# Kernel tuning notes

Hardware: AMD Instinct MI355X
Metric: run time of the kernel (lower is better)

## Reference

```python
import jax, jax.numpy as jnp
import numpy as np
from jax import lax

_GRAY = jnp.array([0.299, 0.587, 0.114], dtype=jnp.float32)  # cv2 RGB2GRAY weights


def _conv(x, w, b):
    # x: [B,C,H,W], w: [O,I,kh,kw], SAME padding (matches padding=k//2 for odd k)
    y = lax.conv_general_dilated(x, w, (1, 1), 'SAME',
                                 dimension_numbers=('NCHW', 'OIHW', 'NCHW'))
    return y + b[None, :, None, None]


def _maxpool2(x):
    return lax.reduce_window(x, -jnp.inf, lax.max, (1, 1, 2, 2), (1, 1, 2, 2), 'VALID')


def _resize_bilinear(img, out_h, out_w):
    # cv2.resize INTER_LINEAR semantics: half-pixel-centered bilinear sampling, edge clamped
    B, C, H, W = img.shape
    ys = jnp.clip((jnp.arange(out_h, dtype=jnp.float32) + 0.5) * (H / out_h) - 0.5, 0.0, H - 1)
    xs = jnp.clip((jnp.arange(out_w, dtype=jnp.float32) + 0.5) * (W / out_w) - 0.5, 0.0, W - 1)
    y0 = jnp.floor(ys).astype(jnp.int32)
    x0 = jnp.floor(xs).astype(jnp.int32)
    y1 = jnp.minimum(y0 + 1, H - 1)
    x1 = jnp.minimum(x0 + 1, W - 1)
    wy = (ys - y0.astype(jnp.float32))[None, None, :, None]
    wx = (xs - x0.astype(jnp.float32))[None, None, None, :]
    r0 = img[:, :, y0, :]
    r1 = img[:, :, y1, :]
    rows = r0 * (1.0 - wy) + r1 * wy          # [B,C,out_h,W]
    c0 = rows[:, :, :, x0]
    c1 = rows[:, :, :, x1]
    return c0 * (1.0 - wx) + c1 * wx          # [B,C,out_h,out_w]


def _forward(input, w1, b1, w2, b2, w3, b3, w4, b4, w5, b5):
    x = jax.nn.relu(_conv(input, w1, b1))
    x = _maxpool2(x)
    x = jax.nn.relu(_conv(x, w2, b2))
    x = _maxpool2(x)
    x = jax.nn.relu(_conv(x, w3, b3))
    x = jax.nn.relu(_conv(x, w4, b4))
    x = _conv(x, w5, b5)                       # [B,1,H/4,W/4]
    out_h, out_w = x.shape[2], x.shape[3]
    # rgb2gray path is detached in the original (detach().cpu()): stop_gradient
    gray = jnp.einsum('bchw,c->bhw', lax.stop_gradient(input), _GRAY)[:, None]  # [B,1,H,W]
    gray = _resize_bilinear(gray, out_h, out_w)
    return jax.nn.relu(x + jax.nn.relu(gray))


def setup_inputs() -> dict:
    key = jax.random.key(0)
    ks = jax.random.split(key, 12)
    B, H, W = 8, 768, 1024
    def w(k, shape, fan_in):
        return (jax.random.normal(k, shape, dtype=jnp.float32) / np.sqrt(fan_in)).astype(jnp.float32)
    return {
        'input': jax.random.normal(ks[0], (B, 3, H, W), dtype=jnp.float32),
        'w1': w(ks[1], (20, 3, 7, 7), 3 * 49),  'b1': jnp.zeros((20,), jnp.float32),
        'w2': w(ks[2], (40, 20, 5, 5), 20 * 25), 'b2': jnp.zeros((40,), jnp.float32),
        'w3': w(ks[3], (20, 40, 5, 5), 40 * 25), 'b3': jnp.zeros((20,), jnp.float32),
        'w4': w(ks[4], (10, 20, 5, 5), 20 * 25), 'b4': jnp.zeros((10,), jnp.float32),
        'w5': w(ks[5], (1, 10, 1, 1), 10),       'b5': jnp.zeros((1,), jnp.float32),
    }


def reference(input, w1, b1, w2, b2, w3, b3, w4, b4, w5, b5):
    return _forward(input, w1, b1, w2, b2, w3, b3, w4, b4, w5, b5)
```

## Files before the change

kernel.cpp:

```cpp
#include <hip/hip_runtime.h>


typedef _Float16 half_t;
typedef _Float16 half8 __attribute__((ext_vector_type(8)));
typedef float floatx4 __attribute__((ext_vector_type(4)));

#define IN_H 768
#define IN_W 1024
#define P1H 384
#define P1W 512
#define P2H 192
#define P2W 256

#define OFF_P2 0ULL
#define OFF_P1 44040192ULL
#define OFF_X3 44040192ULL
#define OFF_X4 0ULL
#define OFF_W2 119537664ULL
#define OFF_W3 119691264ULL
#define OFF_W4 119896064ULL
#define OFF_W1 119947264ULL

union PK4 { half_t h[4]; uint2 u; };
union U8 { half8 v; uint2 u[2]; };

__global__ __launch_bounds__(256) void pack_weights(
    const float* __restrict__ w2, const float* __restrict__ w3,
    const float* __restrict__ w4, const float* __restrict__ w1,
    half_t* __restrict__ wp2, half_t* __restrict__ wp3, half_t* __restrict__ wp4,
    half_t* __restrict__ wp1)
{
  int t = blockIdx.x * 256 + threadIdx.x;
  if (t < 38400) {
    int tap = t / 1536, r = t % 1536, oc = r >> 5, c = r & 31;
    float v = (oc < 40 && c < 20) ? w2[(oc * 20 + c) * 25 + tap] : 0.f;
    wp2[t] = (half_t)v;
  } else if (t < 89600) {
    int u = t - 38400;
    int tap = u / 2048, r = u % 2048, oc = r >> 6, c = r & 63;
    float v = (oc < 20 && c < 40) ? w3[(oc * 40 + c) * 25 + tap] : 0.f;
    wp3[u] = (half_t)v;
  } else if (t < 102400) {
    int u = t - 89600;
    int tap = u / 512, r = u % 512, oc = r >> 5, c = r & 31;
    float v = (oc < 10 && c < 20) ? w4[(oc * 20 + c) * 25 + tap] : 0.f;
    wp4[u] = (half_t)v;
  } else if (t < 109568) {
    int u = t - 102400;
    int ky = u / 1024, r = u % 1024, oc = r >> 5, k = r & 31;
    int kx = k >> 2, c = k & 3;
    float v = (oc < 20 && c < 3 && kx < 7) ? w1[((oc * 3 + c) * 7 + ky) * 7 + kx] : 0.f;
    wp1[u] = (half_t)v;
  }
}

__global__ __launch_bounds__(256) void conv1_mfma(
    const float* __restrict__ in, const half_t* __restrict__ wp,
    const float* __restrict__ bias, half_t* __restrict__ P1)
{
  __shared__ __align__(16) half_t ltile[38 * 40 * 4];
  const int b = blockIdx.z, ty0 = blockIdx.y * 32, tx0 = blockIdx.x * 32;
  const int tid = threadIdx.x;
  const int HW1 = IN_H * IN_W;

  const float* p0 = in + (size_t)b * 3 * HW1;
  const bool interior = (blockIdx.x >= 1) && (blockIdx.x <= 30) &&
                        (blockIdx.y >= 1) && (blockIdx.y <= 22);
  if (interior) {
    for (int i = tid; i < 380; i += 256) {
      int r = i / 10, c4 = i - r * 10;
      const float* pr = p0 + (size_t)(ty0 - 3 + r) * IN_W + (tx0 - 4 + 4 * c4);
      float4 v0 = *(const float4*)(pr);
      float4 v1 = *(const float4*)(pr + HW1);
      float4 v2 = *(const float4*)(pr + 2 * HW1);
      PK4 a0, a1, a2, a3;
      a0.h[0] = (half_t)v0.x; a0.h[1] = (half_t)v1.x; a0.h[2] = (half_t)v2.x; a0.h[3] = (half_t)0.f;
      a1.h[0] = (half_t)v0.y; a1.h[1] = (half_t)v1.y; a1.h[2] = (half_t)v2.y; a1.h[3] = (half_t)0.f;
      a2.h[0] = (half_t)v0.z; a2.h[1] = (half_t)v1.z; a2.h[2] = (half_t)v2.z; a2.h[3] = (half_t)0.f;
      a3.h[0] = (half_t)v0.w; a3.h[1] = (half_t)v1.w; a3.h[2] = (half_t)v2.w; a3.h[3] = (half_t)0.f;
      uint4* dst = (uint4*)(ltile + (r * 40 + 4 * c4) * 4);
      dst[0] = make_uint4(a0.u.x, a0.u.y, a1.u.x, a1.u.y);
      dst[1] = make_uint4(a2.u.x, a2.u.y, a3.u.x, a3.u.y);
    }
  } else {
    for (int i = tid; i < 1520; i += 256) {
      int r = i / 40, c = i - r * 40;
      int gy = ty0 - 3 + r, gx = tx0 - 4 + c;
      float v0 = 0.f, v1 = 0.f, v2 = 0.f;
      if (gy >= 0 && gy < IN_H && (unsigned)gx < (unsigned)IN_W) {
        size_t o = (size_t)gy * IN_W + gx;
        v0 = p0[o];
        v1 = p0[o + HW1];
        v2 = p0[o + 2 * HW1];
      }
      PK4 pk;
      pk.h[0] = (half_t)v0; pk.h[1] = (half_t)v1;
      pk.h[2] = (half_t)v2; pk.h[3] = (half_t)0.f;
      *(uint2*)(ltile + (r * 40 + c) * 4) = pk.u;
    }
  }
  __syncthreads();

  const int wv = tid >> 6, ln = tid & 63, q = ln >> 4, nl = ln & 15;
  const int cbase = (2 * nl + 2 * q + 1) * 4;
  const half_t* wA = wp + nl * 32 + q * 8;

  floatx4 bv[2];
  #pragma unroll
  for (int mt = 0; mt < 2; ++mt)
    #pragma unroll
    for (int r = 0; r < 4; ++r) {
      int oc = mt * 16 + q * 4 + r;
      bv[mt][r] = (oc < 20) ? bias[oc] : 0.f;
    }
  const int pc = (tx0 >> 1) + nl;

  #pragma unroll
  for (int p = 0; p < 2; ++p) {
    const int rbase = p * 16 + 4 * wv;
    U8 frag[4][2];
    #pragma unroll
    for (int d = 0; d < 4; ++d) {
      const half_t* rp = ltile + (rbase + d) * 160 + cbase;
      #pragma unroll
      for (int phx = 0; phx < 2; ++phx) {
        frag[d][phx].u[0] = *(const uint2*)(rp + phx * 4);
        frag[d][phx].u[1] = *(const uint2*)(rp + phx * 4 + 4);
      }
    }
    half8 Abuf[2][2];
    Abuf[0][0] = *(const half8*)(wA);
    Abuf[0][1] = *(const half8*)(wA + 512);
    floatx4 acc[2][8];
    #pragma unroll
    for (int mt = 0; mt < 2; ++mt)
      #pragma unroll
      for (int j = 0; j < 8; ++j) acc[mt][j] = (floatx4){0.f, 0.f, 0.f, 0.f};

    #pragma unroll
    for (int ky = 0; ky < 7; ++ky) {
      if (ky < 6) {
        Abuf[(ky + 1) & 1][0] = *(const half8*)(wA + (ky + 1) * 1024);
        Abuf[(ky + 1) & 1][1] = *(const half8*)(wA + (ky + 1) * 1024 + 512);
      }
      #pragma unroll
      for (int j = 0; j < 8; ++j) {
        const int g = j >> 2, ph = j & 3, phy = ph >> 1, phx = ph & 1;
        half8 B = frag[(2 * g + phy + ky) & 3][phx].v;
        acc[0][j] = __builtin_amdgcn_mfma_f32_16x16x32_f16(Abuf[ky & 1][0], B, acc[0][j], 0, 0, 0);
        acc[1][j] = __builtin_amdgcn_mfma_f32_16x16x32_f16(Abuf[ky & 1][1], B, acc[1][j], 0, 0, 0);
      }
      if (ky < 6) {
        const half_t* rp = ltile + (rbase + ky + 4) * 160 + cbase;
        #pragma unroll
        for (int phx = 0; phx < 2; ++phx) {
          frag[ky & 3][phx].u[0] = *(const uint2*)(rp + phx * 4);
          frag[ky & 3][phx].u[1] = *(const uint2*)(rp + phx * 4 + 4);
        }
      }
    }

    const int pr0 = (ty0 >> 1) + 8 * p + 2 * wv;
    #pragma unroll
    for (int g = 0; g < 2; ++g) {
      size_t pxbase = (((size_t)b * P1H + pr0 + g) * P1W + pc) * 24;
      PK4 pk0;
      #pragma unroll
      for (int r = 0; r < 4; ++r) {
        float x = fmaxf(fmaxf(acc[0][g * 4 + 0][r], acc[0][g * 4 + 1][r]),
                        fmaxf(acc[0][g * 4 + 2][r], acc[0][g * 4 + 3][r]));
        pk0.h[r] = (half_t)fmaxf(x + bv[0][r], 0.f);
      }
      *(uint2*)(P1 + pxbase + q * 4) = pk0.u;
      if (q < 2) {
        PK4 pk1;
        #pragma unroll
        for (int r = 0; r < 4; ++r) {
          float x = fmaxf(fmaxf(acc[1][g * 4 + 0][r], acc[1][g * 4 + 1][r]),
                          fmaxf(acc[1][g * 4 + 2][r], acc[1][g * 4 + 3][r]));
          pk1.h[r] = (half_t)fmaxf(x + bv[1][r], 0.f);
        }
        *(uint2*)(P1 + pxbase + 16 + q * 4) = pk1.u;
      }
    }
  }
}

__global__ __launch_bounds__(256, 2) void conv2_mfma(
    const half_t* __restrict__ P1, const half_t* __restrict__ wp,
    const float* __restrict__ bias, half_t* __restrict__ P2)
{
  __shared__ __align__(16) half_t lin[20 * 36 * 24 + 16];
  const int b = blockIdx.z, ty0 = blockIdx.y * 16, tx0 = blockIdx.x * 32;
  const int tid = threadIdx.x;
  if (tid < 16) lin[20 * 36 * 24 + tid] = (half_t)0.f;
  for (int i = tid; i < 2160; i += 256) {
    int px = i / 3, part = i - px * 3;
    int row = px / 36, col = px - row * 36;
    int gy = ty0 - 2 + row, gx = tx0 - 2 + col;
    uint4 v = make_uint4(0, 0, 0, 0);
    if (gy >= 0 && gy < P1H && (unsigned)gx < (unsigned)P1W)
      v = *(const uint4*)(P1 + (((size_t)b * P1H + gy) * P1W + gx) * 24 + part * 8);
    *(uint4*)(lin + px * 24 + part * 8) = v;
  }
  __syncthreads();

  const int wv = tid >> 6, ln = tid & 63, q = ln >> 4, nl = ln & 15;
  const int cbase = 2 * nl * 24 + q * 8;
  half8 frag[4][6];
  #pragma unroll
  for (int d = 0; d < 4; ++d) {
    const half_t* rp = lin + (4 * wv + d) * 864 + cbase;
    #pragma unroll
    for (int c = 0; c < 6; ++c) frag[d][c] = *(const half8*)(rp + c * 24);
  }
  const half_t* wA = wp + nl * 32 + q * 8;
  half8 Abuf[2][3];
  #pragma unroll
  for (int mt = 0; mt < 3; ++mt) Abuf[0][mt] = *(const half8*)(wA + mt * 512);
  floatx4 acc[3][8];
  #pragma unroll
  for (int mt = 0; mt < 3; ++mt)
    #pragma unroll
    for (int j = 0; j < 8; ++j) acc[mt][j] = (floatx4){0.f, 0.f, 0.f, 0.f};

  #pragma unroll
  for (int ky = 0; ky < 5; ++ky) {
    #pragma unroll
    for (int kx = 0; kx < 5; ++kx) {
      const int tap = ky * 5 + kx;
      if (tap < 24) {
        #pragma unroll
        for (int mt = 0; mt < 3; ++mt)
          Abuf[(tap + 1) & 1][mt] = *(const half8*)(wA + (tap + 1) * 1536 + mt * 512);
      }
      #pragma unroll
      for (int j = 0; j < 8; ++j) {
        const int g = j >> 2, ph = j & 3, phy = ph >> 1, phx = ph & 1;
        half8 B = frag[(2 * g + phy + ky) & 3][kx + phx];
        acc[0][j] = __builtin_amdgcn_mfma_f32_16x16x32_f16(Abuf[tap & 1][0], B, acc[0][j], 0, 0, 0);
        acc[1][j] = __builtin_amdgcn_mfma_f32_16x16x32_f16(Abuf[tap & 1][1], B, acc[1][j], 0, 0, 0);
        acc[2][j] = __builtin_amdgcn_mfma_f32_16x16x32_f16(Abuf[tap & 1][2], B, acc[2][j], 0, 0, 0);
      }
    }
    if (ky < 4) {
      const half_t* rp = lin + (4 * wv + ky + 4) * 864 + cbase;
      #pragma unroll
      for (int c = 0; c < 6; ++c) frag[ky & 3][c] = *(const half8*)(rp + c * 24);
    }
  }

  floatx4 bv[3];
  #pragma unroll
  for (int mt = 0; mt < 3; ++mt)
    #pragma unroll
    for (int r = 0; r < 4; ++r) {
      int oc = mt * 16 + q * 4 + r;
      bv[mt][r] = (oc < 40) ? bias[oc] : 0.f;
    }
  const int pr0 = (ty0 >> 1) + 2 * wv;
  const int pc = (tx0 >> 1) + nl;
  #pragma unroll
  for (int g = 0; g < 2; ++g) {
    size_t pxbase = (((size_t)b * P2H + pr0 + g) * P2W + pc) * 56;
    #pragma unroll
    for (int mt = 0; mt < 3; ++mt) {
      PK4 pk;
      #pragma unroll
      for (int r = 0; r < 4; ++r) {
        float x = fmaxf(fmaxf(acc[mt][g * 4 + 0][r], acc[mt][g * 4 + 1][r]),
                        fmaxf(acc[mt][g * 4 + 2][r], acc[mt][g * 4 + 3][r]));
        pk.h[r] = (half_t)fmaxf(x + bv[mt][r], 0.f);
      }
      *(uint2*)(P2 + pxbase + mt * 16 + q * 4) = pk.u;
    }
    if (q == 0)
      *(uint4*)(P2 + pxbase + 48) = make_uint4(0, 0, 0, 0);
  }
}

__global__ __launch_bounds__(256, 2) void conv3_mfma(
    const half_t* __restrict__ P2, const half_t* __restrict__ wp,
    const float* __restrict__ bias, half_t* __restrict__ X3)
{
  __shared__ __align__(16) half_t lin[12 * 36 * 56 + 16];
  const int b = blockIdx.z, ty0 = blockIdx.y * 8, tx0 = blockIdx.x * 32;
  const int tid = threadIdx.x;
  if (tid < 16) lin[12 * 36 * 56 + tid] = (half_t)0.f;
  for (int i = tid; i < 3024; i += 256) {
    int px = i / 7, part = i - px * 7;
    int row = px / 36, col = px - row * 36;
    int gy = ty0 - 2 + row, gx = tx0 - 2 + col;
    uint4 v = make_uint4(0, 0, 0, 0);
    if (gy >= 0 && gy < P2H && (unsigned)gx < (unsigned)P2W)
      v = *(const uint4*)(P2 + (((size_t)b * P2H + gy) * P2W + gx) * 56 + part * 8);
    *(uint4*)(lin + px * 56 + part * 8) = v;
  }
  __syncthreads();

  const int wv = tid >> 6, ln = tid & 63, q = ln >> 4, nl = ln & 15;
  const int cbase = 2 * nl * 56 + q * 8;
  half8 frag[2][6][2];
  #pragma unroll
  for (int c = 0; c < 6; ++c)
    #pragma unroll
    for (int cb = 0; cb < 2; ++cb) {
      frag[0][c][cb] = *(const half8*)(lin + (2 * wv + 0) * 2016 + cbase + c * 56 + cb * 32);
      frag[1][c][cb] = *(const half8*)(lin + (2 * wv + 1) * 2016 + cbase + c * 56 + cb * 32);
    }
  const half_t* wA = wp + nl * 64 + q * 8;
  half8 Abuf[2][2][2];
  #pragma unroll
  for (int mt = 0; mt < 2; ++mt)
    #pragma unroll
    for (int cb = 0; cb < 2; ++cb)
      Abuf[0][mt][cb] = *(const half8*)(wA + mt * 1024 + cb * 32);
  floatx4 acc[2][4];
  #pragma unroll
  for (int mt = 0; mt < 2; ++mt)
    #pragma unroll
    for (int j = 0; j < 4; ++j) acc[mt][j] = (floatx4){0.f, 0.f, 0.f, 0.f};

  #pragma unroll
  for (int ky = 0; ky < 5; ++ky) {
    #pragma unroll
    for (int kx = 0; kx < 5; ++kx) {
      const int tap = ky * 5 + kx;
      if (tap < 24) {
        #pragma unroll
        for (int mt = 0; mt < 2; ++mt)
          #pragma unroll
          for (int cb = 0; cb < 2; ++cb)
            Abuf[(tap + 1) & 1][mt][cb] =
                *(const half8*)(wA + (tap + 1) * 2048 + mt * 1024 + cb * 32);
      }
      #pragma unroll
      for (int cb = 0; cb < 2; ++cb)
        #pragma unroll
        for (int j = 0; j < 4; ++j) {
          const int phy = j >> 1, phx = j & 1;
          half8 B = frag[(ky + phy) & 1][kx + phx][cb];
          acc[0][j] = __builtin_amdgcn_mfma_f32_16x16x32_f16(Abuf[tap & 1][0][cb], B, acc[0][j], 0, 0, 0);
          acc[1][j] = __builtin_amdgcn_mfma_f32_16x16x32_f16(Abuf[tap & 1][1][cb], B, acc[1][j], 0, 0, 0);
        }
    }
    if (ky < 4) {
      const half_t* rp = lin + (2 * wv + ky + 2) * 2016 + cbase;
      #pragma unroll
      for (int c = 0; c < 6; ++c)
        #pragma unroll
        for (int cb = 0; cb < 2; ++cb)
          frag[ky & 1][c][cb] = *(const half8*)(rp + c * 56 + cb * 32);
    }
  }

  floatx4 bv[2];
  #pragma unroll
  for (int mt = 0; mt < 2; ++mt)
    #pragma unroll
    for (int r = 0; r < 4; ++r) {
      int oc = mt * 16 + q * 4 + r;
      bv[mt][r] = (oc < 20) ? bias[oc] : 0.f;
    }
  #pragma unroll
  for (int j = 0; j < 4; ++j) {
    const int phy = j >> 1, phx = j & 1;
    int y = ty0 + 2 * wv + phy, x = tx0 + 2 * nl + phx;
    size_t pxbase = (((size_t)b * P2H + y) * P2W + x) * 24;
    #pragma unroll
    for (int mt = 0; mt < 2; ++mt) {
      if (mt == 1 && q >= 2) continue;
      floatx4 v = acc[mt][j];
      PK4 pk;
      #pragma unroll
      for (int r = 0; r < 4; ++r) pk.h[r] = (half_t)fmaxf(v[r] + bv[mt][r], 0.f);
      *(uint2*)(X3 + pxbase + mt * 16 + q * 4) = pk.u;
    }
  }
}

__global__ __launch_bounds__(256, 2) void conv4_mfma(
    const half_t* __restrict__ X3, const half_t* __restrict__ wp,
    const float* __restrict__ bias, float* __restrict__ X4)
{
  __shared__ __align__(16) half_t lin[20 * 36 * 24 + 16];
  const int b = blockIdx.z, ty0 = blockIdx.y * 16, tx0 = blockIdx.x * 32;
  const int tid = threadIdx.x;
  if (tid < 16) lin[20 * 36 * 24 + tid] = (half_t)0.f;
  for (int i = tid; i < 2160; i += 256) {
    int px = i / 3, part = i - px * 3;
    int row = px / 36, col = px - row * 36;
    int gy = ty0 - 2 + row, gx = tx0 - 2 + col;
    uint4 v = make_uint4(0, 0, 0, 0);
    if (gy >= 0 && gy < P2H && (unsigned)gx < (unsigned)P2W)
      v = *(const uint4*)(X3 + (((size_t)b * P2H + gy) * P2W + gx) * 24 + part * 8);
    *(uint4*)(lin + px * 24 + part * 8) = v;
  }
  __syncthreads();

  const int wv = tid >> 6, ln = tid & 63, q = ln >> 4, nl = ln & 15;
  const int cbase = 2 * nl * 24 + q * 8;
  half8 frag[4][6];
  #pragma unroll
  for (int d = 0; d < 4; ++d) {
    const half_t* rp = lin + (4 * wv + d) * 864 + cbase;
    #pragma unroll
    for (int c = 0; c < 6; ++c) frag[d][c] = *(const half8*)(rp + c * 24);
  }
  const half_t* wA = wp + nl * 32 + q * 8;
  half8 Abuf[2];
  Abuf[0] = *(const half8*)(wA);
  floatx4 acc[8];
  #pragma unroll
  for (int j = 0; j < 8; ++j) acc[j] = (floatx4){0.f, 0.f, 0.f, 0.f};

  #pragma unroll
  for (int ky = 0; ky < 5; ++ky) {
    #pragma unroll
    for (int kx = 0; kx < 5; ++kx) {
      const int tap = ky * 5 + kx;
      if (tap < 24) Abuf[(tap + 1) & 1] = *(const half8*)(wA + (tap + 1) * 512);
      #pragma unroll
      for (int j = 0; j < 8; ++j) {
        const int g = j >> 2, ph = j & 3, phy = ph >> 1, phx = ph & 1;
        half8 B = frag[(2 * g + phy + ky) & 3][kx + phx];
        acc[j] = __builtin_amdgcn_mfma_f32_16x16x32_f16(Abuf[tap & 1], B, acc[j], 0, 0, 0);
      }
    }
    if (ky < 4) {
      const half_t* rp = lin + (4 * wv + ky + 4) * 864 + cbase;
      #pragma unroll
      for (int c = 0; c < 6; ++c) frag[ky & 3][c] = *(const half8*)(rp + c * 24);
    }
  }

  float bv[4];
  #pragma unroll
  for (int r = 0; r < 4; ++r) {
    int oc = q * 4 + r;
    bv[r] = (oc < 10) ? bias[oc] : 0.f;
  }
  #pragma unroll
  for (int j = 0; j < 8; ++j) {
    const int g = j >> 2, ph = j & 3, phy = ph >> 1, phx = ph & 1;
    int y = ty0 + 4 * wv + 2 * g + phy, x = tx0 + 2 * nl + phx;
    float* dst = X4 + (((size_t)b * P2H + y) * P2W + x) * 10;
    floatx4 v = acc[j];
    float r0 = fmaxf(v[0] + bv[0], 0.f), r1 = fmaxf(v[1] + bv[1], 0.f);
    float r2 = fmaxf(v[2] + bv[2], 0.f), r3 = fmaxf(v[3] + bv[3], 0.f);
    if (q < 2) {
      *(float2*)(dst + q * 4)     = make_float2(r0, r1);
      *(float2*)(dst + q * 4 + 2) = make_float2(r2, r3);
    } else if (q == 2) {
      *(float2*)(dst + 8) = make_float2(r0, r1);
    }
  }
}

__global__ __launch_bounds__(256) void conv5_res(
    const float* __restrict__ X4, const float* __restrict__ w5,
    const float* __restrict__ b5, const float* __restrict__ in,
    float* __restrict__ out)
{
  const int idx = blockIdx.x * 256 + threadIdx.x;
  const int j = idx & 255;
  const int bi = idx >> 8;
  const int i = bi % 192;
  const int b = bi / 192;
  const float* xp = X4 + (((size_t)b * P2H + i) * P2W + j) * 10;
  float sum = b5[0];
  #pragma unroll
  for (int c = 0; c < 10; ++c) sum += w5[c] * xp[c];
  const int r0 = 4 * i + 1;
  const size_t cb = (size_t)r0 * IN_W + 4 * j;
  float g = 0.f;
  #pragma unroll
  for (int ch = 0; ch < 3; ++ch) {
    const float coef = (ch == 0) ? 0.299f : ((ch == 1) ? 0.587f : 0.114f);
    const float* q = in + ((size_t)b * 3 + ch) * IN_H * IN_W;
    float4 a = *(const float4*)(q + cb);
    float4 d = *(const float4*)(q + cb + IN_W);
    g += coef * (a.y + a.z + d.y + d.z);
  }
  g *= 0.25f;
  out[idx] = fmaxf(sum + fmaxf(g, 0.f), 0.f);
}

extern "C" void kernel_launch(void* const* d_in, const int* in_sizes, int n_in,
                              void* d_out, int out_size, void* d_ws, size_t ws_size,
                              hipStream_t stream) {
  const float* input = (const float*)d_in[0];
  const float* w1 = (const float*)d_in[1];  const float* b1 = (const float*)d_in[2];
  const float* w2 = (const float*)d_in[3];  const float* b2 = (const float*)d_in[4];
  const float* w3 = (const float*)d_in[5];  const float* b3 = (const float*)d_in[6];
  const float* w4 = (const float*)d_in[7];  const float* b4 = (const float*)d_in[8];
  const float* w5 = (const float*)d_in[9];  const float* b5 = (const float*)d_in[10];
  float* out = (float*)d_out;
  char* ws = (char*)d_ws;

  half_t* P2h = (half_t*)(ws + OFF_P2);
  half_t* P1h = (half_t*)(ws + OFF_P1);
  half_t* X3h = (half_t*)(ws + OFF_X3);
  float*  X4f = (float*)(ws + OFF_X4);
  half_t* wp2 = (half_t*)(ws + OFF_W2);
  half_t* wp3 = (half_t*)(ws + OFF_W3);
  half_t* wp4 = (half_t*)(ws + OFF_W4);
  half_t* wp1 = (half_t*)(ws + OFF_W1);

  pack_weights<<<432, 256, 0, stream>>>(w2, w3, w4, w1, wp2, wp3, wp4, wp1);
  conv1_mfma<<<dim3(32, 24, 8), 256, 0, stream>>>(input, wp1, b1, P1h);
  conv2_mfma<<<dim3(16, 24, 8), 256, 0, stream>>>(P1h, wp2, b2, P2h);
  conv3_mfma<<<dim3(8, 24, 8), 256, 0, stream>>>(P2h, wp3, b3, X3h);
  conv4_mfma<<<dim3(8, 12, 8), 256, 0, stream>>>(X3h, wp4, b4, X4f);
  conv5_res<<<1536, 256, 0, stream>>>(X4f, w5, b5, input, out);
}
```

Baseline: 385.3 us.

## Use async global-to-LDS loads with double-buffered multi-tile loops in conv2-4

Replaces the register round-trip staging of halo tiles in conv2, conv3 and conv4 with global_load_lds direct-to-LDS copies. Out-of-bounds lanes read from a small zeroed buffer that pack_weights now fills. conv2 and conv4 now process several row tiles per block (4 and 2) with double-buffered LDS, so the next tile is prefetched while MFMA work runs on the current one. The grids are shrunk to match. The cost is double the LDS per block, which may lower occupancy, and fewer blocks in flight.

```diff
diff --git a/kernel.cpp b/kernel.cpp
--- a/kernel.cpp
+++ b/kernel.cpp
@@ -20,15 +20,21 @@
 #define OFF_W3 119691264ULL
 #define OFF_W4 119896064ULL
 #define OFF_W1 119947264ULL
+#define OFF_ZP 119961600ULL
 
 union PK4 { half_t h[4]; uint2 u; };
 union U8 { half8 v; uint2 u[2]; };
+
+#define GLD16(gsrc, ldst)                                          \
+  __builtin_amdgcn_global_load_lds(                                \
+      (const __attribute__((address_space(1))) void*)(gsrc),       \
+      (__attribute__((address_space(3))) void*)(ldst), 16, 0, 0)
 
 __global__ __launch_bounds__(256) void pack_weights(
     const float* __restrict__ w2, const float* __restrict__ w3,
     const float* __restrict__ w4, const float* __restrict__ w1,
     half_t* __restrict__ wp2, half_t* __restrict__ wp3, half_t* __restrict__ wp4,
-    half_t* __restrict__ wp1)
+    half_t* __restrict__ wp1, half_t* __restrict__ zp)
 {
   int t = blockIdx.x * 256 + threadIdx.x;
   if (t < 38400) {
@@ -51,6 +57,8 @@
     int kx = k >> 2, c = k & 3;
     float v = (oc < 20 && c < 3 && kx < 7) ? w1[((oc * 3 + c) * 7 + ky) * 7 + kx] : 0.f;
     wp1[u] = (half_t)v;
+  } else if (t < 109824) {
+    zp[t - 109568] = (half_t)0.f;
   }
 }
 
@@ -188,68 +196,31 @@
 
 __global__ __launch_bounds__(256, 2) void conv2_mfma(
     const half_t* __restrict__ P1, const half_t* __restrict__ wp,
-    const float* __restrict__ bias, half_t* __restrict__ P2)
+    const float* __restrict__ bias, half_t* __restrict__ P2,
+    const half_t* __restrict__ zp)
 {
-  __shared__ __align__(16) half_t lin[20 * 36 * 24 + 16];
-  const int b = blockIdx.z, ty0 = blockIdx.y * 16, tx0 = blockIdx.x * 32;
+  __shared__ __align__(16) half_t lin[2 * 18432];
+  const int b = blockIdx.z, ty_base = blockIdx.y * 64, tx0 = blockIdx.x * 32;
   const int tid = threadIdx.x;
-  if (tid < 16) lin[20 * 36 * 24 + tid] = (half_t)0.f;
-  for (int i = tid; i < 2160; i += 256) {
-    int px = i / 3, part = i - px * 3;
-    int row = px / 36, col = px - row * 36;
-    int gy = ty0 - 2 + row, gx = tx0 - 2 + col;
-    uint4 v = make_uint4(0, 0, 0, 0);
-    if (gy >= 0 && gy < P1H && (unsigned)gx < (unsigned)P1W)
-      v = *(const uint4*)(P1 + (((size_t)b * P1H + gy) * P1W + gx) * 24 + part * 8);
-    *(uint4*)(lin + px * 24 + part * 8) = v;
-  }
-  __syncthreads();
-
   const int wv = tid >> 6, ln = tid & 63, q = ln >> 4, nl = ln & 15;
+
+  auto stage = [&](int bufsel, int sty0) {
+    half_t* Lb = lin + bufsel * 18432;
+    #pragma unroll
+    for (int r = 0; r < 9; ++r) {
+      int i = r * 256 + tid;
+      int px = i / 3, part = i - px * 3;
+      int row = px / 36, col = px - row * 36;
+      int gy = sty0 - 2 + row, gx = tx0 - 2 + col;
+      const half_t* src = zp;
+      if (i < 2160 && (unsigned)gy < (unsigned)P1H && (unsigned)gx < (unsigned)P1W)
+        src = P1 + (((size_t)b * P1H + gy) * P1W + gx) * 24 + part * 8;
+      GLD16(src, Lb + (size_t)(r * 256 + wv * 64) * 8);
+    }
+  };
+
   const int cbase = 2 * nl * 24 + q * 8;
-  half8 frag[4][6];
-  #pragma unroll
-  for (int d = 0; d < 4; ++d) {
-    const half_t* rp = lin + (4 * wv + d) * 864 + cbase;
-    #pragma unroll
-    for (int c = 0; c < 6; ++c) frag[d][c] = *(const half8*)(rp + c * 24);
-  }
   const half_t* wA = wp + nl * 32 + q * 8;
-  half8 Abuf[2][3];
-  #pragma unroll
-  for (int mt = 0; mt < 3; ++mt) Abuf[0][mt] = *(const half8*)(wA + mt * 512);
-  floatx4 acc[3][8];
-  #pragma unroll
-  for (int mt = 0; mt < 3; ++mt)
-    #pragma unroll
-    for (int j = 0; j < 8; ++j) acc[mt][j] = (floatx4){0.f, 0.f, 0.f, 0.f};
-
-  #pragma unroll
-  for (int ky = 0; ky < 5; ++ky) {
-    #pragma unroll
-    for (int kx = 0; kx < 5; ++kx) {
-      const int tap = ky * 5 + kx;
-      if (tap < 24) {
-        #pragma unroll
-        for (int mt = 0; mt < 3; ++mt)
-          Abuf[(tap + 1) & 1][mt] = *(const half8*)(wA + (tap + 1) * 1536 + mt * 512);
-      }
-      #pragma unroll
-      for (int j = 0; j < 8; ++j) {
-        const int g = j >> 2, ph = j & 3, phy = ph >> 1, phx = ph & 1;
-        half8 B = frag[(2 * g + phy + ky) & 3][kx + phx];
-        acc[0][j] = __builtin_amdgcn_mfma_f32_16x16x32_f16(Abuf[tap & 1][0], B, acc[0][j], 0, 0, 0);
-        acc[1][j] = __builtin_amdgcn_mfma_f32_16x16x32_f16(Abuf[tap & 1][1], B, acc[1][j], 0, 0, 0);
-        acc[2][j] = __builtin_amdgcn_mfma_f32_16x16x32_f16(Abuf[tap & 1][2], B, acc[2][j], 0, 0, 0);
-      }
-    }
-    if (ky < 4) {
-      const half_t* rp = lin + (4 * wv + ky + 4) * 864 + cbase;
-      #pragma unroll
-      for (int c = 0; c < 6; ++c) frag[ky & 3][c] = *(const half8*)(rp + c * 24);
-    }
-  }
-
   floatx4 bv[3];
   #pragma unroll
   for (int mt = 0; mt < 3; ++mt)
@@ -258,47 +229,104 @@
       int oc = mt * 16 + q * 4 + r;
       bv[mt][r] = (oc < 40) ? bias[oc] : 0.f;
     }
-  const int pr0 = (ty0 >> 1) + 2 * wv;
   const int pc = (tx0 >> 1) + nl;
-  #pragma unroll
-  for (int g = 0; g < 2; ++g) {
-    size_t pxbase = (((size_t)b * P2H + pr0 + g) * P2W + pc) * 56;
-    #pragma unroll
-    for (int mt = 0; mt < 3; ++mt) {
-      PK4 pk;
-      #pragma unroll
-      for (int r = 0; r < 4; ++r) {
-        float x = fmaxf(fmaxf(acc[mt][g * 4 + 0][r], acc[mt][g * 4 + 1][r]),
-                        fmaxf(acc[mt][g * 4 + 2][r], acc[mt][g * 4 + 3][r]));
-        pk.h[r] = (half_t)fmaxf(x + bv[mt][r], 0.f);
-      }
-      *(uint2*)(P2 + pxbase + mt * 16 + q * 4) = pk.u;
-    }
-    if (q == 0)
-      *(uint4*)(P2 + pxbase + 48) = make_uint4(0, 0, 0, 0);
+
+  stage(0, ty_base);
+  __syncthreads();
+
+  #pragma unroll 1
+  for (int p = 0; p < 4; ++p) {
+    if (p < 3) stage((p + 1) & 1, ty_base + (p + 1) * 16);
+    const half_t* L = lin + (p & 1) * 18432;
+    const int ty0 = ty_base + p * 16;
+
+    half8 frag[4][6];
+    #pragma unroll
+    for (int d = 0; d < 4; ++d) {
+      const half_t* rp = L + (4 * wv + d) * 864 + cbase;
+      #pragma unroll
+      for (int c = 0; c < 6; ++c) frag[d][c] = *(const half8*)(rp + c * 24);
+    }
+    half8 Abuf[2][3];
+    #pragma unroll
+    for (int mt = 0; mt < 3; ++mt) Abuf[0][mt] = *(const half8*)(wA + mt * 512);
+    floatx4 acc[3][8];
+    #pragma unroll
+    for (int mt = 0; mt < 3; ++mt)
+      #pragma unroll
+      for (int j = 0; j < 8; ++j) acc[mt][j] = (floatx4){0.f, 0.f, 0.f, 0.f};
+
+    #pragma unroll
+    for (int ky = 0; ky < 5; ++ky) {
+      #pragma unroll
+      for (int kx = 0; kx < 5; ++kx) {
+        const int tap = ky * 5 + kx;
+        if (tap < 24) {
+          #pragma unroll
+          for (int mt = 0; mt < 3; ++mt)
+            Abuf[(tap + 1) & 1][mt] = *(const half8*)(wA + (tap + 1) * 1536 + mt * 512);
+        }
+        #pragma unroll
+        for (int j = 0; j < 8; ++j) {
+          const int g = j >> 2, ph = j & 3, phy = ph >> 1, phx = ph & 1;
+          half8 B = frag[(2 * g + phy + ky) & 3][kx + phx];
+          acc[0][j] = __builtin_amdgcn_mfma_f32_16x16x32_f16(Abuf[tap & 1][0], B, acc[0][j], 0, 0, 0);
+          acc[1][j] = __builtin_amdgcn_mfma_f32_16x16x32_f16(Abuf[tap & 1][1], B, acc[1][j], 0, 0, 0);
+          acc[2][j] = __builtin_amdgcn_mfma_f32_16x16x32_f16(Abuf[tap & 1][2], B, acc[2][j], 0, 0, 0);
+        }
+      }
+      if (ky < 4) {
+        const half_t* rp = L + (4 * wv + ky + 4) * 864 + cbase;
+        #pragma unroll
+        for (int c = 0; c < 6; ++c) frag[ky & 3][c] = *(const half8*)(rp + c * 24);
+      }
+    }
+
+    const int pr0 = (ty0 >> 1) + 2 * wv;
+    #pragma unroll
+    for (int g = 0; g < 2; ++g) {
+      size_t pxbase = (((size_t)b * P2H + pr0 + g) * P2W + pc) * 56;
+      #pragma unroll
+      for (int mt = 0; mt < 3; ++mt) {
+        PK4 pk;
+        #pragma unroll
+        for (int r = 0; r < 4; ++r) {
+          float x = fmaxf(fmaxf(acc[mt][g * 4 + 0][r], acc[mt][g * 4 + 1][r]),
+                          fmaxf(acc[mt][g * 4 + 2][r], acc[mt][g * 4 + 3][r]));
+          pk.h[r] = (half_t)fmaxf(x + bv[mt][r], 0.f);
+        }
+        *(uint2*)(P2 + pxbase + mt * 16 + q * 4) = pk.u;
+      }
+      if (q == 0)
+        *(uint4*)(P2 + pxbase + 48) = make_uint4(0, 0, 0, 0);
+    }
+    if (p < 3) __syncthreads();
   }
 }
 
 __global__ __launch_bounds__(256, 2) void conv3_mfma(
     const half_t* __restrict__ P2, const half_t* __restrict__ wp,
-    const float* __restrict__ bias, half_t* __restrict__ X3)
+    const float* __restrict__ bias, half_t* __restrict__ X3,
+    const half_t* __restrict__ zp)
 {
-  __shared__ __align__(16) half_t lin[12 * 36 * 56 + 16];
+  __shared__ __align__(16) half_t lin[24576];
   const int b = blockIdx.z, ty0 = blockIdx.y * 8, tx0 = blockIdx.x * 32;
   const int tid = threadIdx.x;
-  if (tid < 16) lin[12 * 36 * 56 + tid] = (half_t)0.f;
-  for (int i = tid; i < 3024; i += 256) {
+  const int wv = tid >> 6, ln = tid & 63, q = ln >> 4, nl = ln & 15;
+
+  #pragma unroll
+  for (int r = 0; r < 12; ++r) {
+    int i = r * 256 + tid;
     int px = i / 7, part = i - px * 7;
     int row = px / 36, col = px - row * 36;
     int gy = ty0 - 2 + row, gx = tx0 - 2 + col;
-    uint4 v = make_uint4(0, 0, 0, 0);
-    if (gy >= 0 && gy < P2H && (unsigned)gx < (unsigned)P2W)
-      v = *(const uint4*)(P2 + (((size_t)b * P2H + gy) * P2W + gx) * 56 + part * 8);
-    *(uint4*)(lin + px * 56 + part * 8) = v;
+    const half_t* src = zp;
+    if (i < 3024 && (unsigned)gy < (unsigned)P2H && (unsigned)gx < (unsigned)P2W)
+      src = P2 + (((size_t)b * P2H + gy) * P2W + gx) * 56 + part * 8;
+    GLD16(src, lin + (size_t)(r * 256 + wv * 64) * 8);
   }
   __syncthreads();
 
-  const int wv = tid >> 6, ln = tid & 63, q = ln >> 4, nl = ln & 15;
   const int cbase = 2 * nl * 56 + q * 8;
   half8 frag[2][6][2];
   #pragma unroll
@@ -381,79 +409,96 @@
 
 __global__ __launch_bounds__(256, 2) void conv4_mfma(
     const half_t* __restrict__ X3, const half_t* __restrict__ wp,
-    const float* __restrict__ bias, float* __restrict__ X4)
+    const float* __restrict__ bias, float* __restrict__ X4,
+    const half_t* __restrict__ zp)
 {
-  __shared__ __align__(16) half_t lin[20 * 36 * 24 + 16];
-  const int b = blockIdx.z, ty0 = blockIdx.y * 16, tx0 = blockIdx.x * 32;
+  __shared__ __align__(16) half_t lin[2 * 18432];
+  const int b = blockIdx.z, ty_base = blockIdx.y * 32, tx0 = blockIdx.x * 32;
   const int tid = threadIdx.x;
-  if (tid < 16) lin[20 * 36 * 24 + tid] = (half_t)0.f;
-  for (int i = tid; i < 2160; i += 256) {
-    int px = i / 3, part = i - px * 3;
-    int row = px / 36, col = px - row * 36;
-    int gy = ty0 - 2 + row, gx = tx0 - 2 + col;
-    uint4 v = make_uint4(0, 0, 0, 0);
-    if (gy >= 0 && gy < P2H && (unsigned)gx < (unsigned)P2W)
-      v = *(const uint4*)(X3 + (((size_t)b * P2H + gy) * P2W + gx) * 24 + part * 8);
-    *(uint4*)(lin + px * 24 + part * 8) = v;
-  }
-  __syncthreads();
-
   const int wv = tid >> 6, ln = tid & 63, q = ln >> 4, nl = ln & 15;
+
+  auto stage = [&](int bufsel, int sty0) {
+    half_t* Lb = lin + bufsel * 18432;
+    #pragma unroll
+    for (int r = 0; r < 9; ++r) {
+      int i = r * 256 + tid;
+      int px = i / 3, part = i - px * 3;
+      int row = px / 36, col = px - row * 36;
+      int gy = sty0 - 2 + row, gx = tx0 - 2 + col;
+      const half_t* src = zp;
+      if (i < 2160 && (unsigned)gy < (unsigned)P2H && (unsigned)gx < (unsigned)P2W)
+        src = X3 + (((size_t)b * P2H + gy) * P2W + gx) * 24 + part * 8;
+      GLD16(src, Lb + (size_t)(r * 256 + wv * 64) * 8);
+    }
+  };
+
   const int cbase = 2 * nl * 24 + q * 8;
-  half8 frag[4][6];
-  #pragma unroll
-  for (int d = 0; d < 4; ++d) {
-    const half_t* rp = lin + (4 * wv + d) * 864 + cbase;
-    #pragma unroll
-    for (int c = 0; c < 6; ++c) frag[d][c] = *(const half8*)(rp + c * 24);
-  }
   const half_t* wA = wp + nl * 32 + q * 8;
-  half8 Abuf[2];
-  Abuf[0] = *(const half8*)(wA);
-  floatx4 acc[8];
-  #pragma unroll
-  for (int j = 0; j < 8; ++j) acc[j] = (floatx4){0.f, 0.f, 0.f, 0.f};
-
-  #pragma unroll
-  for (int ky = 0; ky < 5; ++ky) {
-    #pragma unroll
-    for (int kx = 0; kx < 5; ++kx) {
-      const int tap = ky * 5 + kx;
-      if (tap < 24) Abuf[(tap + 1) & 1] = *(const half8*)(wA + (tap + 1) * 512);
-      #pragma unroll
-      for (int j = 0; j < 8; ++j) {
-        const int g = j >> 2, ph = j & 3, phy = ph >> 1, phx = ph & 1;
-        half8 B = frag[(2 * g + phy + ky) & 3][kx + phx];
-        acc[j] = __builtin_amdgcn_mfma_f32_16x16x32_f16(Abuf[tap & 1], B, acc[j], 0, 0, 0);
-      }
-    }
-    if (ky < 4) {
-      const half_t* rp = lin + (4 * wv + ky + 4) * 864 + cbase;
-      #pragma unroll
-      for (int c = 0; c < 6; ++c) frag[ky & 3][c] = *(const half8*)(rp + c * 24);
-    }
-  }
-
   float bv[4];
   #pragma unroll
   for (int r = 0; r < 4; ++r) {
     int oc = q * 4 + r;
     bv[r] = (oc < 10) ? bias[oc] : 0.f;
   }
-  #pragma unroll
-  for (int j = 0; j < 8; ++j) {
-    const int g = j >> 2, ph = j & 3, phy = ph >> 1, phx = ph & 1;
-    int y = ty0 + 4 * wv + 2 * g + phy, x = tx0 + 2 * nl + phx;
-    float* dst = X4 + (((size_t)b * P2H + y) * P2W + x) * 10;
-    floatx4 v = acc[j];
-    float r0 = fmaxf(v[0] + bv[0], 0.f), r1 = fmaxf(v[1] + bv[1], 0.f);
-    float r2 = fmaxf(v[2] + bv[2], 0.f), r3 = fmaxf(v[3] + bv[3], 0.f);
-    if (q < 2) {
-      *(float2*)(dst + q * 4)     = make_float2(r0, r1);
-      *(float2*)(dst + q * 4 + 2) = make_float2(r2, r3);
-    } else if (q == 2) {
-      *(float2*)(dst + 8) = make_float2(r0, r1);
-    }
+
+  stage(0, ty_base);
+  __syncthreads();
+
+  #pragma unroll 1
+  for (int p = 0; p < 2; ++p) {
+    if (p < 1) stage(1, ty_base + 16);
+    const half_t* L = lin + (p & 1) * 18432;
+    const int ty0 = ty_base + p * 16;
+
+    half8 frag[4][6];
+    #pragma unroll
+    for (int d = 0; d < 4; ++d) {
+      const half_t* rp = L + (4 * wv + d) * 864 + cbase;
+      #pragma unroll
+      for (int c = 0; c < 6; ++c) frag[d][c] = *(const half8*)(rp + c * 24);
+    }
+    half8 Abuf[2];
+    Abuf[0] = *(const half8*)(wA);
+    floatx4 acc[8];
+    #pragma unroll
+    for (int j = 0; j < 8; ++j) acc[j] = (floatx4){0.f, 0.f, 0.f, 0.f};
+
+    #pragma unroll
+    for (int ky = 0; ky < 5; ++ky) {
+      #pragma unroll
+      for (int kx = 0; kx < 5; ++kx) {
+        const int tap = ky * 5 + kx;
+        if (tap < 24) Abuf[(tap + 1) & 1] = *(const half8*)(wA + (tap + 1) * 512);
+        #pragma unroll
+        for (int j = 0; j < 8; ++j) {
+          const int g = j >> 2, ph = j & 3, phy = ph >> 1, phx = ph & 1;
+          half8 B = frag[(2 * g + phy + ky) & 3][kx + phx];
+          acc[j] = __builtin_amdgcn_mfma_f32_16x16x32_f16(Abuf[tap & 1], B, acc[j], 0, 0, 0);
+        }
+      }
+      if (ky < 4) {
+        const half_t* rp = L + (4 * wv + ky + 4) * 864 + cbase;
+        #pragma unroll
+        for (int c = 0; c < 6; ++c) frag[ky & 3][c] = *(const half8*)(rp + c * 24);
+      }
+    }
+
+    #pragma unroll
+    for (int j = 0; j < 8; ++j) {
+      const int g = j >> 2, ph = j & 3, phy = ph >> 1, phx = ph & 1;
+      int y = ty0 + 4 * wv + 2 * g + phy, x = tx0 + 2 * nl + phx;
+      float* dst = X4 + (((size_t)b * P2H + y) * P2W + x) * 10;
+      floatx4 v = acc[j];
+      float r0 = fmaxf(v[0] + bv[0], 0.f), r1 = fmaxf(v[1] + bv[1], 0.f);
+      float r2 = fmaxf(v[2] + bv[2], 0.f), r3 = fmaxf(v[3] + bv[3], 0.f);
+      if (q < 2) {
+        *(float2*)(dst + q * 4)     = make_float2(r0, r1);
+        *(float2*)(dst + q * 4 + 2) = make_float2(r2, r3);
+      } else if (q == 2) {
+        *(float2*)(dst + 8) = make_float2(r0, r1);
+      }
+    }
+    if (p < 1) __syncthreads();
   }
 }
 
@@ -506,11 +551,12 @@
   half_t* wp3 = (half_t*)(ws + OFF_W3);
   half_t* wp4 = (half_t*)(ws + OFF_W4);
   half_t* wp1 = (half_t*)(ws + OFF_W1);
-
-  pack_weights<<<432, 256, 0, stream>>>(w2, w3, w4, w1, wp2, wp3, wp4, wp1);
+  half_t* zph = (half_t*)(ws + OFF_ZP);
+
+  pack_weights<<<432, 256, 0, stream>>>(w2, w3, w4, w1, wp2, wp3, wp4, wp1, zph);
   conv1_mfma<<<dim3(32, 24, 8), 256, 0, stream>>>(input, wp1, b1, P1h);
-  conv2_mfma<<<dim3(16, 24, 8), 256, 0, stream>>>(P1h, wp2, b2, P2h);
-  conv3_mfma<<<dim3(8, 24, 8), 256, 0, stream>>>(P2h, wp3, b3, X3h);
-  conv4_mfma<<<dim3(8, 12, 8), 256, 0, stream>>>(X3h, wp4, b4, X4f);
+  conv2_mfma<<<dim3(16, 6, 8), 256, 0, stream>>>(P1h, wp2, b2, P2h, zph);
+  conv3_mfma<<<dim3(8, 24, 8), 256, 0, stream>>>(P2h, wp3, b3, X3h, zph);
+  conv4_mfma<<<dim3(8, 6, 8), 256, 0, stream>>>(X3h, wp4, b4, X4f, zph);
   conv5_res<<<1536, 256, 0, stream>>>(X4f, w5, b5, input, out);
 }
```

Result: slower. 886.6 us (+130.1%).

## Make conv2/conv4 persistent over row tiles with double-buffered LDS prefetch

Applied to the files above, without the earlier changes.

conv2 and conv4 now process several 16-row tiles per block (four and two respectively) instead of one. While the current tile is being computed, the next tile's halo is loaded from global memory into registers, then written into a second LDS buffer. The intent is to hide global load latency behind MFMA work and cut the launch and prologue cost per block. In exchange LDS use doubles (about 69KB per block), register pressure rises from the staging registers, and the grids shrink, which lowers the number of blocks available to fill the CUs.

```diff
diff --git a/kernel.cpp b/kernel.cpp
--- a/kernel.cpp
+++ b/kernel.cpp
@@ -190,66 +190,43 @@
     const half_t* __restrict__ P1, const half_t* __restrict__ wp,
     const float* __restrict__ bias, half_t* __restrict__ P2)
 {
-  __shared__ __align__(16) half_t lin[20 * 36 * 24 + 16];
-  const int b = blockIdx.z, ty0 = blockIdx.y * 16, tx0 = blockIdx.x * 32;
+  #define C2_BUF 17296
+  __shared__ __align__(16) half_t lin[2 * C2_BUF];
+  const int b = blockIdx.z, ty_base = blockIdx.y * 64, tx0 = blockIdx.x * 32;
   const int tid = threadIdx.x;
-  if (tid < 16) lin[20 * 36 * 24 + tid] = (half_t)0.f;
-  for (int i = tid; i < 2160; i += 256) {
-    int px = i / 3, part = i - px * 3;
-    int row = px / 36, col = px - row * 36;
-    int gy = ty0 - 2 + row, gx = tx0 - 2 + col;
-    uint4 v = make_uint4(0, 0, 0, 0);
-    if (gy >= 0 && gy < P1H && (unsigned)gx < (unsigned)P1W)
-      v = *(const uint4*)(P1 + (((size_t)b * P1H + gy) * P1W + gx) * 24 + part * 8);
-    *(uint4*)(lin + px * 24 + part * 8) = v;
-  }
-  __syncthreads();
-
   const int wv = tid >> 6, ln = tid & 63, q = ln >> 4, nl = ln & 15;
+
+  if (tid < 16) {
+    lin[17280 + tid] = (half_t)0.f;
+    lin[C2_BUF + 17280 + tid] = (half_t)0.f;
+  }
+
+  auto stage_load = [&](int sty0, uint4* stg) {
+    #pragma unroll
+    for (int r = 0; r < 9; ++r) {
+      int i = r * 256 + tid;
+      uint4 v = make_uint4(0, 0, 0, 0);
+      if (i < 2160) {
+        int px = i / 3, part = i - px * 3;
+        int row = px / 36, col = px - row * 36;
+        int gy = sty0 - 2 + row, gx = tx0 - 2 + col;
+        if ((unsigned)gy < (unsigned)P1H && (unsigned)gx < (unsigned)P1W)
+          v = *(const uint4*)(P1 + (((size_t)b * P1H + gy) * P1W + gx) * 24 + part * 8);
+      }
+      stg[r] = v;
+    }
+  };
+  auto stage_write = [&](int bufsel, const uint4* stg) {
+    half_t* Lb = lin + bufsel * C2_BUF;
+    #pragma unroll
+    for (int r = 0; r < 9; ++r) {
+      int i = r * 256 + tid;
+      if (i < 2160) *(uint4*)(Lb + i * 8) = stg[r];
+    }
+  };
+
   const int cbase = 2 * nl * 24 + q * 8;
-  half8 frag[4][6];
-  #pragma unroll
-  for (int d = 0; d < 4; ++d) {
-    const half_t* rp = lin + (4 * wv + d) * 864 + cbase;
-    #pragma unroll
-    for (int c = 0; c < 6; ++c) frag[d][c] = *(const half8*)(rp + c * 24);
-  }
   const half_t* wA = wp + nl * 32 + q * 8;
-  half8 Abuf[2][3];
-  #pragma unroll
-  for (int mt = 0; mt < 3; ++mt) Abuf[0][mt] = *(const half8*)(wA + mt * 512);
-  floatx4 acc[3][8];
-  #pragma unroll
-  for (int mt = 0; mt < 3; ++mt)
-    #pragma unroll
-    for (int j = 0; j < 8; ++j) acc[mt][j] = (floatx4){0.f, 0.f, 0.f, 0.f};
-
-  #pragma unroll
-  for (int ky = 0; ky < 5; ++ky) {
-    #pragma unroll
-    for (int kx = 0; kx < 5; ++kx) {
-      const int tap = ky * 5 + kx;
-      if (tap < 24) {
-        #pragma unroll
-        for (int mt = 0; mt < 3; ++mt)
-          Abuf[(tap + 1) & 1][mt] = *(const half8*)(wA + (tap + 1) * 1536 + mt * 512);
-      }
-      #pragma unroll
-      for (int j = 0; j < 8; ++j) {
-        const int g = j >> 2, ph = j & 3, phy = ph >> 1, phx = ph & 1;
-        half8 B = frag[(2 * g + phy + ky) & 3][kx + phx];
-        acc[0][j] = __builtin_amdgcn_mfma_f32_16x16x32_f16(Abuf[tap & 1][0], B, acc[0][j], 0, 0, 0);
-        acc[1][j] = __builtin_amdgcn_mfma_f32_16x16x32_f16(Abuf[tap & 1][1], B, acc[1][j], 0, 0, 0);
-        acc[2][j] = __builtin_amdgcn_mfma_f32_16x16x32_f16(Abuf[tap & 1][2], B, acc[2][j], 0, 0, 0);
-      }
-    }
-    if (ky < 4) {
-      const half_t* rp = lin + (4 * wv + ky + 4) * 864 + cbase;
-      #pragma unroll
-      for (int c = 0; c < 6; ++c) frag[ky & 3][c] = *(const half8*)(rp + c * 24);
-    }
-  }
-
   floatx4 bv[3];
   #pragma unroll
   for (int mt = 0; mt < 3; ++mt)
@@ -258,25 +235,88 @@
       int oc = mt * 16 + q * 4 + r;
       bv[mt][r] = (oc < 40) ? bias[oc] : 0.f;
     }
-  const int pr0 = (ty0 >> 1) + 2 * wv;
   const int pc = (tx0 >> 1) + nl;
-  #pragma unroll
-  for (int g = 0; g < 2; ++g) {
-    size_t pxbase = (((size_t)b * P2H + pr0 + g) * P2W + pc) * 56;
-    #pragma unroll
-    for (int mt = 0; mt < 3; ++mt) {
-      PK4 pk;
-      #pragma unroll
-      for (int r = 0; r < 4; ++r) {
-        float x = fmaxf(fmaxf(acc[mt][g * 4 + 0][r], acc[mt][g * 4 + 1][r]),
-                        fmaxf(acc[mt][g * 4 + 2][r], acc[mt][g * 4 + 3][r]));
-        pk.h[r] = (half_t)fmaxf(x + bv[mt][r], 0.f);
-      }
-      *(uint2*)(P2 + pxbase + mt * 16 + q * 4) = pk.u;
-    }
-    if (q == 0)
-      *(uint4*)(P2 + pxbase + 48) = make_uint4(0, 0, 0, 0);
-  }
+
+  {
+    uint4 stg[9];
+    stage_load(ty_base, stg);
+    stage_write(0, stg);
+  }
+  __syncthreads();
+
+  #pragma unroll 1
+  for (int p = 0; p < 4; ++p) {
+    uint4 stg[9];
+    if (p < 3) stage_load(ty_base + (p + 1) * 16, stg);
+    const half_t* L = lin + (p & 1) * C2_BUF;
+    const int ty0 = ty_base + p * 16;
+
+    half8 frag[4][6];
+    #pragma unroll
+    for (int d = 0; d < 4; ++d) {
+      const half_t* rp = L + (4 * wv + d) * 864 + cbase;
+      #pragma unroll
+      for (int c = 0; c < 6; ++c) frag[d][c] = *(const half8*)(rp + c * 24);
+    }
+    half8 Abuf[2][3];
+    #pragma unroll
+    for (int mt = 0; mt < 3; ++mt) Abuf[0][mt] = *(const half8*)(wA + mt * 512);
+    floatx4 acc[3][8];
+    #pragma unroll
+    for (int mt = 0; mt < 3; ++mt)
+      #pragma unroll
+      for (int j = 0; j < 8; ++j) acc[mt][j] = (floatx4){0.f, 0.f, 0.f, 0.f};
+
+    #pragma unroll
+    for (int ky = 0; ky < 5; ++ky) {
+      #pragma unroll
+      for (int kx = 0; kx < 5; ++kx) {
+        const int tap = ky * 5 + kx;
+        if (tap < 24) {
+          #pragma unroll
+          for (int mt = 0; mt < 3; ++mt)
+            Abuf[(tap + 1) & 1][mt] = *(const half8*)(wA + (tap + 1) * 1536 + mt * 512);
+        }
+        #pragma unroll
+        for (int j = 0; j < 8; ++j) {
+          const int g = j >> 2, ph = j & 3, phy = ph >> 1, phx = ph & 1;
+          half8 B = frag[(2 * g + phy + ky) & 3][kx + phx];
+          acc[0][j] = __builtin_amdgcn_mfma_f32_16x16x32_f16(Abuf[tap & 1][0], B, acc[0][j], 0, 0, 0);
+          acc[1][j] = __builtin_amdgcn_mfma_f32_16x16x32_f16(Abuf[tap & 1][1], B, acc[1][j], 0, 0, 0);
+          acc[2][j] = __builtin_amdgcn_mfma_f32_16x16x32_f16(Abuf[tap & 1][2], B, acc[2][j], 0, 0, 0);
+        }
+      }
+      if (ky < 4) {
+        const half_t* rp = L + (4 * wv + ky + 4) * 864 + cbase;
+        #pragma unroll
+        for (int c = 0; c < 6; ++c) frag[ky & 3][c] = *(const half8*)(rp + c * 24);
+      }
+    }
+
+    const int pr0 = (ty0 >> 1) + 2 * wv;
+    #pragma unroll
+    for (int g = 0; g < 2; ++g) {
+      size_t pxbase = (((size_t)b * P2H + pr0 + g) * P2W + pc) * 56;
+      #pragma unroll
+      for (int mt = 0; mt < 3; ++mt) {
+        PK4 pk;
+        #pragma unroll
+        for (int r = 0; r < 4; ++r) {
+          float x = fmaxf(fmaxf(acc[mt][g * 4 + 0][r], acc[mt][g * 4 + 1][r]),
+                          fmaxf(acc[mt][g * 4 + 2][r], acc[mt][g * 4 + 3][r]));
+          pk.h[r] = (half_t)fmaxf(x + bv[mt][r], 0.f);
+        }
+        *(uint2*)(P2 + pxbase + mt * 16 + q * 4) = pk.u;
+      }
+      if (q == 0)
+        *(uint4*)(P2 + pxbase + 48) = make_uint4(0, 0, 0, 0);
+    }
+    if (p < 3) {
+      stage_write((p + 1) & 1, stg);
+      __syncthreads();
+    }
+  }
+  #undef C2_BUF
 }
 
 __global__ __launch_bounds__(256, 2) void conv3_mfma(
@@ -383,78 +423,118 @@
     const half_t* __restrict__ X3, const half_t* __restrict__ wp,
     const float* __restrict__ bias, float* __restrict__ X4)
 {
-  __shared__ __align__(16) half_t lin[20 * 36 * 24 + 16];
-  const int b = blockIdx.z, ty0 = blockIdx.y * 16, tx0 = blockIdx.x * 32;
+  #define C4_BUF 17296
+  __shared__ __align__(16) half_t lin[2 * C4_BUF];
+  const int b = blockIdx.z, ty_base = blockIdx.y * 32, tx0 = blockIdx.x * 32;
   const int tid = threadIdx.x;
-  if (tid < 16) lin[20 * 36 * 24 + tid] = (half_t)0.f;
-  for (int i = tid; i < 2160; i += 256) {
-    int px = i / 3, part = i - px * 3;
-    int row = px / 36, col = px - row * 36;
-    int gy = ty0 - 2 + row, gx = tx0 - 2 + col;
-    uint4 v = make_uint4(0, 0, 0, 0);
-    if (gy >= 0 && gy < P2H && (unsigned)gx < (unsigned)P2W)
-      v = *(const uint4*)(X3 + (((size_t)b * P2H + gy) * P2W + gx) * 24 + part * 8);
-    *(uint4*)(lin + px * 24 + part * 8) = v;
-  }
-  __syncthreads();
-
   const int wv = tid >> 6, ln = tid & 63, q = ln >> 4, nl = ln & 15;
+
+  if (tid < 16) {
+    lin[17280 + tid] = (half_t)0.f;
+    lin[C4_BUF + 17280 + tid] = (half_t)0.f;
+  }
+
+  auto stage_load = [&](int sty0, uint4* stg) {
+    #pragma unroll
+    for (int r = 0; r < 9; ++r) {
+      int i = r * 256 + tid;
+      uint4 v = make_uint4(0, 0, 0, 0);
+      if (i < 2160) {
+        int px = i / 3, part = i - px * 3;
+        int row = px / 36, col = px - row * 36;
+        int gy = sty0 - 2 + row, gx = tx0 - 2 + col;
+        if ((unsigned)gy < (unsigned)P2H && (unsigned)gx < (unsigned)P2W)
+          v = *(const uint4*)(X3 + (((size_t)b * P2H + gy) * P2W + gx) * 24 + part * 8);
+      }
+      stg[r] = v;
+    }
+  };
+  auto stage_write = [&](int bufsel, const uint4* stg) {
+    half_t* Lb = lin + bufsel * C4_BUF;
+    #pragma unroll
+    for (int r = 0; r < 9; ++r) {
+      int i = r * 256 + tid;
+      if (i < 2160) *(uint4*)(Lb + i * 8) = stg[r];
+    }
+  };
+
   const int cbase = 2 * nl * 24 + q * 8;
-  half8 frag[4][6];
-  #pragma unroll
-  for (int d = 0; d < 4; ++d) {
-    const half_t* rp = lin + (4 * wv + d) * 864 + cbase;
-    #pragma unroll
-    for (int c = 0; c < 6; ++c) frag[d][c] = *(const half8*)(rp + c * 24);
-  }
   const half_t* wA = wp + nl * 32 + q * 8;
-  half8 Abuf[2];
-  Abuf[0] = *(const half8*)(wA);
-  floatx4 acc[8];
-  #pragma unroll
-  for (int j = 0; j < 8; ++j) acc[j] = (floatx4){0.f, 0.f, 0.f, 0.f};
-
-  #pragma unroll
-  for (int ky = 0; ky < 5; ++ky) {
-    #pragma unroll
-    for (int kx = 0; kx < 5; ++kx) {
-      const int tap = ky * 5 + kx;
-      if (tap < 24) Abuf[(tap + 1) & 1] = *(const half8*)(wA + (tap + 1) * 512);
-      #pragma unroll
-      for (int j = 0; j < 8; ++j) {
-        const int g = j >> 2, ph = j & 3, phy = ph >> 1, phx = ph & 1;
-        half8 B = frag[(2 * g + phy + ky) & 3][kx + phx];
-        acc[j] = __builtin_amdgcn_mfma_f32_16x16x32_f16(Abuf[tap & 1], B, acc[j], 0, 0, 0);
-      }
-    }
-    if (ky < 4) {
-      const half_t* rp = lin + (4 * wv + ky + 4) * 864 + cbase;
-      #pragma unroll
-      for (int c = 0; c < 6; ++c) frag[ky & 3][c] = *(const half8*)(rp + c * 24);
-    }
-  }
-
   float bv[4];
   #pragma unroll
   for (int r = 0; r < 4; ++r) {
     int oc = q * 4 + r;
     bv[r] = (oc < 10) ? bias[oc] : 0.f;
   }
-  #pragma unroll
-  for (int j = 0; j < 8; ++j) {
-    const int g = j >> 2, ph = j & 3, phy = ph >> 1, phx = ph & 1;
-    int y = ty0 + 4 * wv + 2 * g + phy, x = tx0 + 2 * nl + phx;
-    float* dst = X4 + (((size_t)b * P2H + y) * P2W + x) * 10;
-    floatx4 v = acc[j];
-    float r0 = fmaxf(v[0] + bv[0], 0.f), r1 = fmaxf(v[1] + bv[1], 0.f);
-    float r2 = fmaxf(v[2] + bv[2], 0.f), r3 = fmaxf(v[3] + bv[3], 0.f);
-    if (q < 2) {
-      *(float2*)(dst + q * 4)     = make_float2(r0, r1);
-      *(float2*)(dst + q * 4 + 2) = make_float2(r2, r3);
-    } else if (q == 2) {
-      *(float2*)(dst + 8) = make_float2(r0, r1);
-    }
-  }
+
+  {
+    uint4 stg[9];
+    stage_load(ty_base, stg);
+    stage_write(0, stg);
+  }
+  __syncthreads();
+
+  #pragma unroll 1
+  for (int p = 0; p < 2; ++p) {
+    uint4 stg[9];
+    if (p < 1) stage_load(ty_base + 16, stg);
+    const half_t* L = lin + (p & 1) * C4_BUF;
+    const int ty0 = ty_base + p * 16;
+
+    half8 frag[4][6];
+    #pragma unroll
+    for (int d = 0; d < 4; ++d) {
+      const half_t* rp = L + (4 * wv + d) * 864 + cbase;
+      #pragma unroll
+      for (int c = 0; c < 6; ++c) frag[d][c] = *(const half8*)(rp + c * 24);
+    }
+    half8 Abuf[2];
+    Abuf[0] = *(const half8*)(wA);
+    floatx4 acc[8];
+    #pragma unroll
+    for (int j = 0; j < 8; ++j) acc[j] = (floatx4){0.f, 0.f, 0.f, 0.f};
+
+    #pragma unroll
+    for (int ky = 0; ky < 5; ++ky) {
+      #pragma unroll
+      for (int kx = 0; kx < 5; ++kx) {
+        const int tap = ky * 5 + kx;
+        if (tap < 24) Abuf[(tap + 1) & 1] = *(const half8*)(wA + (tap + 1) * 512);
+        #pragma unroll
+        for (int j = 0; j < 8; ++j) {
+          const int g = j >> 2, ph = j & 3, phy = ph >> 1, phx = ph & 1;
+          half8 B = frag[(2 * g + phy + ky) & 3][kx + phx];
+          acc[j] = __builtin_amdgcn_mfma_f32_16x16x32_f16(Abuf[tap & 1], B, acc[j], 0, 0, 0);
+        }
+      }
+      if (ky < 4) {
+        const half_t* rp = L + (4 * wv + ky + 4) * 864 + cbase;
+        #pragma unroll
+        for (int c = 0; c < 6; ++c) frag[ky & 3][c] = *(const half8*)(rp + c * 24);
+      }
+    }
+
+    #pragma unroll
+    for (int j = 0; j < 8; ++j) {
+      const int g = j >> 2, ph = j & 3, phy = ph >> 1, phx = ph & 1;
+      int y = ty0 + 4 * wv + 2 * g + phy, x = tx0 + 2 * nl + phx;
+      float* dst = X4 + (((size_t)b * P2H + y) * P2W + x) * 10;
+      floatx4 v = acc[j];
+      float r0 = fmaxf(v[0] + bv[0], 0.f), r1 = fmaxf(v[1] + bv[1], 0.f);
+      float r2 = fmaxf(v[2] + bv[2], 0.f), r3 = fmaxf(v[3] + bv[3], 0.f);
+      if (q < 2) {
+        *(float2*)(dst + q * 4)     = make_float2(r0, r1);
+        *(float2*)(dst + q * 4 + 2) = make_float2(r2, r3);
+      } else if (q == 2) {
+        *(float2*)(dst + 8) = make_float2(r0, r1);
+      }
+    }
+    if (p < 1) {
+      stage_write(1, stg);
+      __syncthreads();
+    }
+  }
+  #undef C4_BUF
 }
 
 __global__ __launch_bounds__(256) void conv5_res(
@@ -509,8 +589,8 @@
 
   pack_weights<<<432, 256, 0, stream>>>(w2, w3, w4, w1, wp2, wp3, wp4, wp1);
   conv1_mfma<<<dim3(32, 24, 8), 256, 0, stream>>>(input, wp1, b1, P1h);
-  conv2_mfma<<<dim3(16, 24, 8), 256, 0, stream>>>(P1h, wp2, b2, P2h);
+  conv2_mfma<<<dim3(16, 6, 8), 256, 0, stream>>>(P1h, wp2, b2, P2h);
   conv3_mfma<<<dim3(8, 24, 8), 256, 0, stream>>>(P2h, wp3, b3, X3h);
-  conv4_mfma<<<dim3(8, 12, 8), 256, 0, stream>>>(X3h, wp4, b4, X4f);
+  conv4_mfma<<<dim3(8, 6, 8), 256, 0, stream>>>(X3h, wp4, b4, X4f);
   conv5_res<<<1536, 256, 0, stream>>>(X4f, w5, b5, input, out);
 }
```

After: 960.6 us. 2.49x slower.
